# Optimization experiments

Measured on AMD Instinct MI355X. Metric: run time of the kernel, lower is better.

## Reference

```python
import jax, jax.numpy as jnp
import numpy as np

B, C, H, W = 4, 256, 64, 64


def conv1x1(x, w, b):
    # x: [B,C,H,W], w: [O,C] (1x1 kernel squeezed), b: [O]
    return jnp.einsum('bchw,oc->bohw', x, w) + b[None, :, None, None]


def setup_inputs() -> dict:
    key = jax.random.key(0)
    ks = jax.random.split(key, 7)
    fuse = jax.random.normal(ks[0], (B, C, H, W), dtype=jnp.float32)
    scale = 0.02
    Wq = jax.random.normal(ks[1], (C, C), dtype=jnp.float32) * scale
    bq = jnp.zeros((C,), dtype=jnp.float32)
    Wk = jax.random.normal(ks[2], (C, C), dtype=jnp.float32) * scale
    bk = jnp.zeros((C,), dtype=jnp.float32)
    Wv = jax.random.normal(ks[3], (C, C), dtype=jnp.float32) * scale
    bv = jnp.zeros((C,), dtype=jnp.float32)
    return {'fuse': fuse, 'Wq': Wq, 'bq': bq, 'Wk': Wk, 'bk': bk, 'Wv': Wv, 'bv': bv}


def reference(fuse, Wq, bq, Wk, bk, Wv, bv):
    b, c, h, w = fuse.shape
    hw = h * w
    scale = 1.0 / (c ** 0.5)
    Q = conv1x1(fuse, Wq, bq).reshape(b, c, hw)          # [B, C, HW]
    K = conv1x1(fuse, Wk, bk).reshape(b, c, hw)          # [B, C, HW]
    # Q_mask: reshape [B,C,HW] -> [B*H, C*W], max over rows -> [1, C*W]
    Q_mask = jnp.max(Q.reshape(b * h, c * w), axis=0, keepdims=True)
    # scores: [B, HW(query), HW(key)]
    scores = jnp.einsum('bcn,bcm->bnm', Q, K) * scale
    # NOTE: softmax over dim=0 (batch axis), faithful to the torch source
    soft = jax.nn.softmax(scores, axis=0)
    m = jnp.max(soft, axis=1)                             # [B, HW]
    m = jnp.max(m.reshape(-1, w), axis=-1, keepdims=True) # [B*H, 1]
    mask = (m @ Q_mask).reshape(b, c, h, w)               # [B*H,1]x[1,C*W]
    V = conv1x1(fuse, Wv, bv)
    return V + V * mask
```

## Files before the change

kernel.cpp:

```cpp
#include <hip/hip_runtime.h>
#include <stdint.h>

#define HW 4096
#define CH 256
#define NB 4

typedef __attribute__((ext_vector_type(8))) short bf16x8;
typedef __attribute__((ext_vector_type(4))) float f32x4;
typedef __attribute__((ext_vector_type(2))) long longx2;
typedef unsigned char u8;

__device__ __forceinline__ ushort f2bf(float f) {
    uint32_t u = __float_as_uint(f);
    u += 0x7fffu + ((u >> 16) & 1u);
    return (ushort)(u >> 16);
}
__device__ __forceinline__ uint fkey(float f) {
    uint b = __float_as_uint(f);
    return ((int)b < 0) ? ~b : (b | 0x80000000u);
}
__device__ __forceinline__ float finv(uint k) {
    uint b = (k & 0x80000000u) ? (k ^ 0x80000000u) : ~k;
    return __uint_as_float(b);
}

__device__ __forceinline__ size_t fragidx(int b, int o, int hw) {
    return ((((size_t)b * 8 + (o >> 5)) * 128 + (hw >> 5)) * 1024)
         + ((((o >> 3) & 3) * 16 + (hw & 15)) * 16)
         + (((hw >> 4) & 1) * 8) + (o & 7);
}

__global__ __launch_bounds__(256) void prep_kernel(
    const float* __restrict__ Wq, const float* __restrict__ Wk,
    const float* __restrict__ Wv,
    ushort* __restrict__ Wq16, ushort* __restrict__ Wk16,
    ushort* __restrict__ Wv16, unsigned int* __restrict__ m2k,
    unsigned int* __restrict__ qmk) {
    int i = blockIdx.x * 256 + threadIdx.x;
    Wq16[i] = f2bf(Wq[i]);
    Wk16[i] = f2bf(Wk[i]);
    Wv16[i] = f2bf(Wv[i]);
    if (i < NB * HW) qmk[i] = 0;
    if (i < NB * 64) m2k[i] = 0;
}

__global__ __launch_bounds__(256) void convQK_kernel(
    const float* __restrict__ fuse,
    const ushort* __restrict__ Wq16, const ushort* __restrict__ Wk16,
    const float* __restrict__ bq, const float* __restrict__ bk,
    u8* __restrict__ Qw8, u8* __restrict__ Kw8,
    unsigned int* __restrict__ qmout) {
    __shared__ __align__(16) ushort WqLs[256][72];
    __shared__ __align__(16) ushort WkLs[256][72];
    __shared__ __align__(16) float tileF[64][65];
    __shared__ __align__(16) ushort Bls[64][72];
    __shared__ float qred[4][4][64];
    const int t = threadIdx.x;
    const int lane = t & 63, w = t >> 6;
    const int hw0 = blockIdx.x * 64;
    const int b = blockIdx.y;
    f32x4 accQ[4][4] = {}, accK[4][4] = {};
    for (int kc = 0; kc < 4; ++kc) {
        __syncthreads();
        #pragma unroll
        for (int i = 0; i < 8; ++i) {
            int q = t + 256 * i;
            int row = q >> 3, c8 = (q & 7) * 8;
            *(int4*)&WqLs[row][c8] =
                *(const int4*)(Wq16 + (size_t)row * CH + kc * 64 + c8);
            *(int4*)&WkLs[row][c8] =
                *(const int4*)(Wk16 + (size_t)row * CH + kc * 64 + c8);
        }
        {
            const int c = t >> 2, q4 = (t & 3) * 16;
            const float* src = fuse + ((size_t)b * CH + kc * 64 + c) * HW + hw0 + q4;
            #pragma unroll
            for (int q = 0; q < 4; ++q) {
                float4 v = *(const float4*)(src + q * 4);
                tileF[c][q4 + q * 4 + 0] = v.x; tileF[c][q4 + q * 4 + 1] = v.y;
                tileF[c][q4 + q * 4 + 2] = v.z; tileF[c][q4 + q * 4 + 3] = v.w;
            }
        }
        __syncthreads();
        #pragma unroll
        for (int rep = 0; rep < 2; ++rep) {
            int u = t + rep * 256;
            int hw = u >> 3, i8 = (u & 7) * 8;
            __align__(16) ushort o8[8];
            #pragma unroll
            for (int k = 0; k < 8; ++k) o8[k] = f2bf(tileF[i8 + k][hw]);
            *(int4*)&Bls[hw][i8] = *(const int4*)o8;
        }
        __syncthreads();
        #pragma unroll
        for (int kk = 0; kk < 2; ++kk) {
            bf16x8 aq[4], ak[4];
            #pragma unroll
            for (int rf = 0; rf < 4; ++rf) {
                aq[rf] = *(const bf16x8*)&WqLs[w * 64 + rf * 16 + (lane & 15)]
                                              [kk * 32 + (lane >> 4) * 8];
                ak[rf] = *(const bf16x8*)&WkLs[w * 64 + rf * 16 + (lane & 15)]
                                              [kk * 32 + (lane >> 4) * 8];
            }
            #pragma unroll
            for (int cf = 0; cf < 4; ++cf) {
                bf16x8 bf_ = *(const bf16x8*)&Bls[cf * 16 + (lane & 15)]
                                                 [kk * 32 + (lane >> 4) * 8];
                #pragma unroll
                for (int rf = 0; rf < 4; ++rf) {
                    accQ[rf][cf] = __builtin_amdgcn_mfma_f32_16x16x32_bf16(
                        aq[rf], bf_, accQ[rf][cf], 0, 0, 0);
                    accK[rf][cf] = __builtin_amdgcn_mfma_f32_16x16x32_bf16(
                        ak[rf], bf_, accK[rf][cf], 0, 0, 0);
                }
            }
        }
    }
    float qmx[4][4];
    #pragma unroll
    for (int cf = 0; cf < 4; ++cf)
        #pragma unroll
        for (int r = 0; r < 4; ++r) qmx[cf][r] = -3.4e38f;
    #pragma unroll
    for (int rf = 0; rf < 4; ++rf) {
        const int ob = w * 64 + rf * 16 + (lane >> 4) * 4;
        #pragma unroll
        for (int cf = 0; cf < 4; ++cf) {
            const int hw = hw0 + cf * 16 + (lane & 15);
            size_t idx = fragidx(b, ob, hw);
            {
                float v0 = accQ[rf][cf][0] + bq[ob + 0];
                float v1 = accQ[rf][cf][1] + bq[ob + 1];
                float v2 = accQ[rf][cf][2] + bq[ob + 2];
                float v3 = accQ[rf][cf][3] + bq[ob + 3];
                int u = __builtin_amdgcn_cvt_pk_fp8_f32(v0, v1, 0, false);
                u = __builtin_amdgcn_cvt_pk_fp8_f32(v2, v3, u, true);
                *(unsigned int*)&Qw8[idx] = (unsigned int)u;
                qmx[cf][0] = fmaxf(qmx[cf][0], v0);
                qmx[cf][1] = fmaxf(qmx[cf][1], v1);
                qmx[cf][2] = fmaxf(qmx[cf][2], v2);
                qmx[cf][3] = fmaxf(qmx[cf][3], v3);
            }
            {
                float v0 = accK[rf][cf][0] + bk[ob + 0];
                float v1 = accK[rf][cf][1] + bk[ob + 1];
                float v2 = accK[rf][cf][2] + bk[ob + 2];
                float v3 = accK[rf][cf][3] + bk[ob + 3];
                int u = __builtin_amdgcn_cvt_pk_fp8_f32(v0, v1, 0, false);
                u = __builtin_amdgcn_cvt_pk_fp8_f32(v2, v3, u, true);
                *(unsigned int*)&Kw8[idx] = (unsigned int)u;
            }
        }
    }
    #pragma unroll
    for (int cf = 0; cf < 4; ++cf)
        #pragma unroll
        for (int r = 0; r < 4; ++r) {
            float v = qmx[cf][r];
            v = fmaxf(v, __shfl_xor(v, 16));
            v = fmaxf(v, __shfl_xor(v, 32));
            qmx[cf][r] = v;
        }
    __syncthreads();
    if (lane < 16) {
        #pragma unroll
        for (int cf = 0; cf < 4; ++cf)
            #pragma unroll
            for (int r = 0; r < 4; ++r)
                qred[w][r][cf * 16 + lane] = qmx[cf][r];
    }
    __syncthreads();
    {
        const int r = t >> 6, h64 = t & 63;
        float v = fmaxf(fmaxf(qred[0][r][h64], qred[1][r][h64]),
                        fmaxf(qred[2][r][h64], qred[3][r][h64]));
        atomicMax(qmout + r * HW + hw0 + h64, fkey(v));
    }
}

__global__ __launch_bounds__(256) void convV_kernel(
    const float* __restrict__ fuse, const ushort* __restrict__ Wv16,
    const float* __restrict__ bv, float* __restrict__ outf,
    const unsigned int* __restrict__ m2key,
    const unsigned int* __restrict__ qmkey) {
    __shared__ __align__(16) ushort Als[256][72];
    __shared__ __align__(16) float tileF[64][65];
    __shared__ __align__(16) ushort Bls[64][72];
    __shared__ float m2s[64];
    const int t = threadIdx.x;
    const int lane = t & 63, w = t >> 6;
    const int hw0 = blockIdx.x * 64;
    const int b = blockIdx.y;
    if (t < 64) m2s[t] = __uint_as_float(m2key[b * 64 + t]);
    f32x4 acc[4][4] = {};
    for (int kc = 0; kc < 4; ++kc) {
        __syncthreads();
        #pragma unroll
        for (int i = 0; i < 8; ++i) {
            int q = t + 256 * i;
            int row = q >> 3, c8 = (q & 7) * 8;
            *(int4*)&Als[row][c8] =
                *(const int4*)(Wv16 + (size_t)row * CH + kc * 64 + c8);
        }
        {
            const int c = t >> 2, q4 = (t & 3) * 16;
            const float* src = fuse + ((size_t)b * CH + kc * 64 + c) * HW + hw0 + q4;
            #pragma unroll
            for (int q = 0; q < 4; ++q) {
                float4 v = *(const float4*)(src + q * 4);
                tileF[c][q4 + q * 4 + 0] = v.x; tileF[c][q4 + q * 4 + 1] = v.y;
                tileF[c][q4 + q * 4 + 2] = v.z; tileF[c][q4 + q * 4 + 3] = v.w;
            }
        }
        __syncthreads();
        #pragma unroll
        for (int rep = 0; rep < 2; ++rep) {
            int u = t + rep * 256;
            int hw = u >> 3, i8 = (u & 7) * 8;
            __align__(16) ushort o8[8];
            #pragma unroll
            for (int k = 0; k < 8; ++k) o8[k] = f2bf(tileF[i8 + k][hw]);
            *(int4*)&Bls[hw][i8] = *(const int4*)o8;
        }
        __syncthreads();
        #pragma unroll
        for (int kk = 0; kk < 2; ++kk) {
            bf16x8 af[4];
            #pragma unroll
            for (int rf = 0; rf < 4; ++rf)
                af[rf] = *(const bf16x8*)&Als[w * 64 + rf * 16 + (lane & 15)]
                                             [kk * 32 + (lane >> 4) * 8];
            #pragma unroll
            for (int cf = 0; cf < 4; ++cf) {
                bf16x8 bf_ = *(const bf16x8*)&Bls[cf * 16 + (lane & 15)]
                                                 [kk * 32 + (lane >> 4) * 8];
                #pragma unroll
                for (int rf = 0; rf < 4; ++rf)
                    acc[rf][cf] = __builtin_amdgcn_mfma_f32_16x16x32_bf16(
                        af[rf], bf_, acc[rf][cf], 0, 0, 0);
            }
        }
    }
    #pragma unroll
    for (int rf = 0; rf < 4; ++rf) {
        const int ob = w * 64 + rf * 16 + (lane >> 4) * 4;
        #pragma unroll
        for (int cf = 0; cf < 4; ++cf) {
            const int hw = hw0 + cf * 16 + (lane & 15);
            const float mv = m2s[ob >> 2];
            #pragma unroll
            for (int r = 0; r < 4; ++r) {
                float vv = acc[rf][cf][r] + bv[ob + r];
                float qm = finv(qmkey[r * HW + hw]);
                outf[((size_t)b * CH + ob + r) * HW + hw] = vv * (1.0f + mv * qm);
            }
        }
    }
}

__global__ __launch_bounds__(256, 2) void scores64(
    const u8* __restrict__ Qw, const u8* __restrict__ Kw,
    unsigned int* __restrict__ m2k) {
    __shared__ __align__(16) f32x4 EX[4][4][64];
    __shared__ float red[4][4];
    const int t = threadIdx.x;
    const int lane = t & 63, w = t >> 6;
    const int bid = blockIdx.x;
    const int xcd = bid & 7, j = bid >> 3;
    const int vn = (xcd & 3) * 16 + (j & 15);
    const int vm = (xcd >> 2) * 32 + (j >> 4);

    const u8* qp = Qw + (((size_t)w * 8) * 128 + vn * 2) * 1024 + lane * 16;
    const u8* kp = Kw + (((size_t)w * 8) * 128 + vm * 2) * 1024 + lane * 16;

    longx2 AQ[8][2], BK[8][2];
    #pragma unroll
    for (int kc = 0; kc < 8; ++kc) {
        #pragma unroll
        for (int p = 0; p < 2; ++p) {
            AQ[kc][p] = *(const longx2*)(qp + (size_t)kc * 131072 + p * 1024);
            BK[kc][p] = *(const longx2*)(kp + (size_t)kc * 131072 + p * 1024);
        }
    }
    __builtin_amdgcn_sched_barrier(0);

    f32x4 acc[4][4] = {};
    #pragma unroll
    for (int kc = 0; kc < 8; ++kc) {
        #pragma unroll
        for (int mf = 0; mf < 4; ++mf) {
            long bf_ = BK[kc][mf >> 1][mf & 1];
            #pragma unroll
            for (int nf = 0; nf < 4; ++nf)
                acc[nf][mf] = __builtin_amdgcn_mfma_f32_16x16x32_fp8_fp8(
                    AQ[kc][nf >> 1][nf & 1], bf_, acc[nf][mf], 0, 0, 0);
        }
    }

    float pmAll[4] = {0.f, 0.f, 0.f, 0.f};
    #pragma unroll
    for (int nf = 0; nf < 4; ++nf) {
        if (nf) __syncthreads();
        #pragma unroll
        for (int mf = 0; mf < 4; ++mf)
            EX[w][mf][lane] = acc[nf][mf];
        __syncthreads();
        f32x4 sv[4];
        #pragma unroll
        for (int b2 = 0; b2 < 4; ++b2)
            sv[b2] = EX[b2][w][lane];
        #pragma unroll
        for (int jj = 0; jj < 4; ++jj) {
            float e0 = __expf(sv[0][jj] * 0.0625f);
            float e1 = __expf(sv[1][jj] * 0.0625f);
            float e2 = __expf(sv[2][jj] * 0.0625f);
            float e3 = __expf(sv[3][jj] * 0.0625f);
            float inv = __fdividef(1.0f, e0 + e1 + e2 + e3);
            pmAll[0] = fmaxf(pmAll[0], e0 * inv);
            pmAll[1] = fmaxf(pmAll[1], e1 * inv);
            pmAll[2] = fmaxf(pmAll[2], e2 * inv);
            pmAll[3] = fmaxf(pmAll[3], e3 * inv);
        }
    }
    #pragma unroll
    for (int off = 32; off >= 1; off >>= 1) {
        pmAll[0] = fmaxf(pmAll[0], __shfl_xor(pmAll[0], off));
        pmAll[1] = fmaxf(pmAll[1], __shfl_xor(pmAll[1], off));
        pmAll[2] = fmaxf(pmAll[2], __shfl_xor(pmAll[2], off));
        pmAll[3] = fmaxf(pmAll[3], __shfl_xor(pmAll[3], off));
    }
    __syncthreads();
    if (lane == 0) {
        #pragma unroll
        for (int b2 = 0; b2 < 4; ++b2) red[w][b2] = pmAll[b2];
    }
    __syncthreads();
    if (t < 4) {
        float v = fmaxf(fmaxf(red[0][t], red[1][t]),
                        fmaxf(red[2][t], red[3][t]));
        atomicMax(m2k + t * 64 + vm, __float_as_uint(v));
    }
}

extern "C" void kernel_launch(void* const* d_in, const int* in_sizes, int n_in,
                              void* d_out, int out_size, void* d_ws, size_t ws_size,
                              hipStream_t stream) {
    const float* fuse = (const float*)d_in[0];
    const float* Wq   = (const float*)d_in[1];
    const float* bq   = (const float*)d_in[2];
    const float* Wk   = (const float*)d_in[3];
    const float* bk   = (const float*)d_in[4];
    const float* Wv   = (const float*)d_in[5];
    const float* bv   = (const float*)d_in[6];
    float* out = (float*)d_out;

    char* ws = (char*)d_ws;
    ushort* Wq16  = (ushort*)(ws);
    ushort* Wk16  = (ushort*)(ws + 131072);
    ushort* Wv16  = (ushort*)(ws + 262144);
    u8*     Qw8   = (u8*)    (ws + 393216);
    u8*     Kw8   = (u8*)    (ws + 4587520);
    unsigned int* QMK = (unsigned int*)(ws + 8781824);
    unsigned int* M2K = (unsigned int*)(ws + 8847360);

    prep_kernel<<<256, 256, 0, stream>>>(Wq, Wk, Wv, Wq16, Wk16, Wv16, M2K, QMK);
    convQK_kernel<<<dim3(64, NB), 256, 0, stream>>>(
        fuse, Wq16, Wk16, bq, bk, Qw8, Kw8, QMK);
    scores64<<<4096, 256, 0, stream>>>(Qw8, Kw8, M2K);
    convV_kernel<<<dim3(64, NB), 256, 0, stream>>>(
        fuse, Wv16, bv, out, M2K, QMK);
}
```

Measured before the change: 74.49 us.

## Make scores blocks persistent over 8 query tiles with K reused and Q prefetched

Each scores block now keeps its K tile in registers and loops over 8 query tiles, cutting the grid from 4096 to 512 blocks. The Q fragments for the next tile are loaded while the current tile's softmax epilogue runs, overlapping loads with compute. This reduces redundant K loads, per-block launch and setup overhead, and atomicMax traffic. In exchange there are fewer blocks to fill the GPU, more registers in use, and a larger shared exchange buffer that could lower occupancy.

```diff
diff --git a/kernel.cpp b/kernel.cpp
--- a/kernel.cpp
+++ b/kernel.cpp
@@ -261,67 +261,78 @@
 __global__ __launch_bounds__(256, 2) void scores64(
     const u8* __restrict__ Qw, const u8* __restrict__ Kw,
     unsigned int* __restrict__ m2k) {
-    __shared__ __align__(16) f32x4 EX[4][4][64];
+    __shared__ __align__(16) f32x4 EX[4][4][4][64];
     __shared__ float red[4][4];
     const int t = threadIdx.x;
     const int lane = t & 63, w = t >> 6;
     const int bid = blockIdx.x;
     const int xcd = bid & 7, j = bid >> 3;
-    const int vn = (xcd & 3) * 16 + (j & 15);
-    const int vm = (xcd >> 2) * 32 + (j >> 4);
-
-    const u8* qp = Qw + (((size_t)w * 8) * 128 + vn * 2) * 1024 + lane * 16;
+    const int vm = xcd * 8 + (j & 7);
+    const int s  = j >> 3;
+
     const u8* kp = Kw + (((size_t)w * 8) * 128 + vm * 2) * 1024 + lane * 16;
-
-    longx2 AQ[8][2], BK[8][2];
-    #pragma unroll
-    for (int kc = 0; kc < 8; ++kc) {
-        #pragma unroll
-        for (int p = 0; p < 2; ++p) {
-            AQ[kc][p] = *(const longx2*)(qp + (size_t)kc * 131072 + p * 1024);
+    const u8* qp0 = Qw + (((size_t)w * 8) * 128 + (s * 8) * 2) * 1024 + lane * 16;
+
+    longx2 BK[8][2];
+    #pragma unroll
+    for (int kc = 0; kc < 8; ++kc)
+        #pragma unroll
+        for (int p = 0; p < 2; ++p)
             BK[kc][p] = *(const longx2*)(kp + (size_t)kc * 131072 + p * 1024);
-        }
-    }
-    __builtin_amdgcn_sched_barrier(0);
-
-    f32x4 acc[4][4] = {};
-    #pragma unroll
-    for (int kc = 0; kc < 8; ++kc) {
-        #pragma unroll
-        for (int mf = 0; mf < 4; ++mf) {
-            long bf_ = BK[kc][mf >> 1][mf & 1];
-            #pragma unroll
-            for (int nf = 0; nf < 4; ++nf)
-                acc[nf][mf] = __builtin_amdgcn_mfma_f32_16x16x32_fp8_fp8(
-                    AQ[kc][nf >> 1][nf & 1], bf_, acc[nf][mf], 0, 0, 0);
-        }
-    }
+
+    longx2 AQ[8][2];
+#define LOADQ(IT)                                                          \
+    _Pragma("unroll") for (int kc = 0; kc < 8; ++kc)                       \
+        _Pragma("unroll") for (int p = 0; p < 2; ++p)                      \
+            AQ[kc][p] = *(const longx2*)(qp0 + (IT) * 2048                 \
+                                         + (size_t)kc * 131072 + p * 1024);
+    LOADQ(0)
 
     float pmAll[4] = {0.f, 0.f, 0.f, 0.f};
     #pragma unroll
-    for (int nf = 0; nf < 4; ++nf) {
-        if (nf) __syncthreads();
-        #pragma unroll
-        for (int mf = 0; mf < 4; ++mf)
-            EX[w][mf][lane] = acc[nf][mf];
-        __syncthreads();
-        f32x4 sv[4];
-        #pragma unroll
-        for (int b2 = 0; b2 < 4; ++b2)
-            sv[b2] = EX[b2][w][lane];
-        #pragma unroll
-        for (int jj = 0; jj < 4; ++jj) {
-            float e0 = __expf(sv[0][jj] * 0.0625f);
-            float e1 = __expf(sv[1][jj] * 0.0625f);
-            float e2 = __expf(sv[2][jj] * 0.0625f);
-            float e3 = __expf(sv[3][jj] * 0.0625f);
-            float inv = __fdividef(1.0f, e0 + e1 + e2 + e3);
-            pmAll[0] = fmaxf(pmAll[0], e0 * inv);
-            pmAll[1] = fmaxf(pmAll[1], e1 * inv);
-            pmAll[2] = fmaxf(pmAll[2], e2 * inv);
-            pmAll[3] = fmaxf(pmAll[3], e3 * inv);
-        }
-    }
+    for (int it = 0; it < 8; ++it) {
+        f32x4 acc[4][4] = {};
+        #pragma unroll
+        for (int kc = 0; kc < 8; ++kc) {
+            #pragma unroll
+            for (int mf = 0; mf < 4; ++mf) {
+                long bf_ = BK[kc][mf >> 1][mf & 1];
+                #pragma unroll
+                for (int nf = 0; nf < 4; ++nf)
+                    acc[nf][mf] = __builtin_amdgcn_mfma_f32_16x16x32_fp8_fp8(
+                        AQ[kc][nf >> 1][nf & 1], bf_, acc[nf][mf], 0, 0, 0);
+            }
+        }
+        if (it + 1 < 8) { LOADQ(it + 1) }
+
+        if (it) __syncthreads();
+        #pragma unroll
+        for (int nf = 0; nf < 4; ++nf)
+            #pragma unroll
+            for (int mf = 0; mf < 4; ++mf)
+                EX[w][nf][mf][lane] = acc[nf][mf];
+        __syncthreads();
+        #pragma unroll
+        for (int nf = 0; nf < 4; ++nf) {
+            f32x4 sv[4];
+            #pragma unroll
+            for (int b2 = 0; b2 < 4; ++b2)
+                sv[b2] = EX[b2][nf][w][lane];
+            #pragma unroll
+            for (int jj = 0; jj < 4; ++jj) {
+                float e0 = __expf(sv[0][jj] * 0.0625f);
+                float e1 = __expf(sv[1][jj] * 0.0625f);
+                float e2 = __expf(sv[2][jj] * 0.0625f);
+                float e3 = __expf(sv[3][jj] * 0.0625f);
+                float inv = __fdividef(1.0f, e0 + e1 + e2 + e3);
+                pmAll[0] = fmaxf(pmAll[0], e0 * inv);
+                pmAll[1] = fmaxf(pmAll[1], e1 * inv);
+                pmAll[2] = fmaxf(pmAll[2], e2 * inv);
+                pmAll[3] = fmaxf(pmAll[3], e3 * inv);
+            }
+        }
+    }
+#undef LOADQ
     #pragma unroll
     for (int off = 32; off >= 1; off >>= 1) {
         pmAll[0] = fmaxf(pmAll[0], __shfl_xor(pmAll[0], off));
@@ -366,7 +377,7 @@
     prep_kernel<<<256, 256, 0, stream>>>(Wq, Wk, Wv, Wq16, Wk16, Wv16, M2K, QMK);
     convQK_kernel<<<dim3(64, NB), 256, 0, stream>>>(
         fuse, Wq16, Wk16, bq, bk, Qw8, Kw8, QMK);
-    scores64<<<4096, 256, 0, stream>>>(Qw8, Kw8, M2K);
+    scores64<<<512, 256, 0, stream>>>(Qw8, Kw8, M2K);
     convV_kernel<<<dim3(64, NB), 256, 0, stream>>>(
         fuse, Wv16, bv, out, M2K, QMK);
 }
```

New measurement: 72.03 us. 1.03x faster.
